# Optimization experiments

Measured on AMD Instinct MI355X. Metric: run time of the kernel, lower is better.

Reference implementation:

```python
import jax, jax.numpy as jnp
import numpy as np

B, T, C_IN, C_HID, C_EMB, K, MAX_DUR = 16, 512, 512, 256, 384, 5, 8
MAX_MEL = T * MAX_DUR  # static upper bound on regulated length (4096)
LRELU_SLOPE = 0.3
PAD = (K - 1) // 2
EPS = 1e-5


def setup_inputs() -> dict:
    key = jax.random.key(0)
    ks = jax.random.split(key, 14)
    s = 0.05
    return {
        "x": jax.random.normal(ks[0], (B, T, C_IN), jnp.float32),
        "x_res": jax.random.normal(ks[1], (B, T, C_IN), jnp.float32),
        "duration_target": jax.random.randint(ks[2], (B, T), 0, MAX_DUR, dtype=jnp.int32),
        "embeddings": jax.random.normal(ks[3], (B, T, C_EMB), jnp.float32),
        "src_mask": jnp.zeros((B, T), jnp.bool_),
        "conv1_w": s * jax.random.normal(ks[4], (K, C_IN, C_HID), jnp.float32),
        "conv1_b": jnp.zeros((C_HID,), jnp.float32),
        "ln1_g": jnp.ones((C_HID,), jnp.float32),
        "ln1_b": jnp.zeros((C_HID,), jnp.float32),
        "conv2_w": s * jax.random.normal(ks[5], (K, C_HID, C_HID), jnp.float32),
        "conv2_b": jnp.zeros((C_HID,), jnp.float32),
        "ln2_g": jnp.ones((C_HID,), jnp.float32),
        "ln2_b": jnp.zeros((C_HID,), jnp.float32),
        "lin_w": s * jax.random.normal(ks[6], (C_HID, 1), jnp.float32),
        "lin_b": jnp.zeros((1,), jnp.float32),
    }


def _conv1d(x, w, b):
    # x: [B, T, Cin], w: [K, Cin, Cout] -> [B, T, Cout] (same padding)
    y = jax.lax.conv_general_dilated(
        x, w, window_strides=(1,), padding=[(PAD, PAD)],
        dimension_numbers=("NWC", "WIO", "NWC"))
    return y + b


def _layer_norm(x, g, b):
    mu = jnp.mean(x, axis=-1, keepdims=True)
    var = jnp.mean(jnp.square(x - mu), axis=-1, keepdims=True)
    return (x - mu) * jax.lax.rsqrt(var + EPS) * g + b


def _duration_predictor(x, mask, c1w, c1b, g1, b1, c2w, c2b, g2, b2, lw, lb):
    h = jax.nn.leaky_relu(_conv1d(x, c1w, c1b), LRELU_SLOPE)
    h = _layer_norm(h, g1, b1)  # dropout is identity at eval
    h = jax.nn.leaky_relu(_conv1d(h, c2w, c2b), LRELU_SLOPE)
    h = _layer_norm(h, g2, b2)
    h = (h @ lw + lb).squeeze(-1)  # [B, T]
    return jnp.where(mask, 0.0, h)


def _length_regulate(x, duration):
    # Fused prefix-sum + gather replacement for the looped expand/cat/pad.
    # token i occupies output frames [cumsum[i-1], cumsum[i])
    cum = jnp.cumsum(duration, axis=1)              # [B, T]
    total = cum[:, -1]                              # [B] mel lengths
    pos = jnp.arange(MAX_MEL, dtype=cum.dtype)      # [MAX_MEL]
    idx = jax.vmap(lambda c: jnp.searchsorted(c, pos, side="right"))(cum)  # [B, MAX_MEL]
    idx = jnp.clip(idx, 0, duration.shape[1] - 1)
    valid = (pos[None, :] < total[:, None])         # [B, MAX_MEL]
    out = jnp.take_along_axis(x, idx[..., None], axis=1)
    out = out * valid[..., None].astype(x.dtype)    # zero-padded past mel_len
    return out, total.astype(jnp.int32)


def reference(x, x_res, duration_target, embeddings, src_mask,
              conv1_w, conv1_b, ln1_g, ln1_b, conv2_w, conv2_b, ln2_g, ln2_b,
              lin_w, lin_b):
    # upsample_train path: x_res is detached before the duration predictor
    x_res = jax.lax.stop_gradient(x_res)
    log_duration_prediction = _duration_predictor(
        x_res, src_mask, conv1_w, conv1_b, ln1_g, ln1_b,
        conv2_w, conv2_b, ln2_g, ln2_b, lin_w, lin_b)
    x_up, _ = _length_regulate(x, duration_target)
    emb_up, _ = _length_regulate(embeddings, duration_target)
    return x_up, log_duration_prediction, emb_up
```

## Files before the change

kernel.cpp:

```cpp
#include <hip/hip_runtime.h>


constexpr int Bn = 16, Tn = 512, CIN1 = 512, CHID = 256, CEMB = 384, MAXMEL = 4096;
constexpr int NROWS = Bn * Tn;
#define LRELU 0.3f
#define EPSV 1e-5f

typedef __attribute__((ext_vector_type(8))) short bf16x8;
typedef __attribute__((ext_vector_type(4))) float f32x4;
typedef __attribute__((ext_vector_type(16))) float f32x16;
typedef unsigned short ushort_t;

static __device__ __forceinline__ ushort_t f2bf(float f) {
  unsigned u = __builtin_bit_cast(unsigned, f);
  unsigned r = (u + 0x7fffu + ((u >> 16) & 1u)) >> 16;
  return (ushort_t)r;
}

__global__ __launch_bounds__(256) void wprep_kernel(const float* __restrict__ w,
                                                    ushort_t* __restrict__ out,
                                                    int CI) {
  const int gid = blockIdx.x * 256 + threadIdx.x;
  const int ksh = gid / (CI * 256);
  const int rem = gid - ksh * CI * 256;
  const int ci = rem >> 8, co = rem & 255;
  const int ci16 = ci >> 4, cob32 = co >> 5;
  const int l = ((ci >> 3) & 1) * 32 + (co & 31);
  const int j = ci & 7;
  const size_t dst = ((size_t)((ksh * (CI / 16) + ci16) * 8 + cob32)) * 512 + l * 8 + j;
  out[dst] = f2bf(w[gid]);
}

template <int CI, bool F32IN>
__global__ __launch_bounds__(256, 2) void conv_mfma_kernel(
    const float* __restrict__ xin,
    const ushort_t* __restrict__ inbf,
    const ushort_t* __restrict__ wB,
    float* __restrict__ hraw) {
  constexpr int NCHUNK = CI / 64;
  constexpr int ROWS = 36, LDSTRIDE = 72;
  __shared__ ushort_t sA[ROWS * LDSTRIDE];

  const int mt = blockIdx.x, ns = blockIdx.y;
  const int b = mt >> 4, t0 = (mt & 15) * 32;
  const int tid = threadIdx.x;
  const int l = tid & 63, nh = tid >> 6;
  const int lm = l & 31, lq = l >> 5;
  const int cob32 = ns * 4 + nh;

  f32x16 acc;
#pragma unroll
  for (int i = 0; i < 16; ++i) acc[i] = 0.f;

  const ushort_t* pB = wB + (size_t)cob32 * 512 + l * 8;

#pragma unroll 1
  for (int chunk = 0; chunk < NCHUNK; ++chunk) {
    {
      const int cibase = chunk * 64;
#pragma unroll 1
      for (int i = 0; i < 5; ++i) {
        const int p = i * 256 + tid;
        if (p < ROWS * 32) {
          const int r = p >> 5, c2 = (p & 31) * 2;
          const int t = t0 - 2 + r;
          unsigned hv = 0;
          if ((unsigned)t < (unsigned)Tn) {
            const size_t src = (size_t)(b * Tn + t) * CI + cibase + c2;
            if (F32IN) {
              const float2 v = *(const float2*)(xin + src);
              hv = (unsigned)f2bf(v.x) | ((unsigned)f2bf(v.y) << 16);
            } else {
              hv = *(const unsigned*)(inbf + src);
            }
          }
          const int sw = ((r >> 3) & 3) << 3;
          *(unsigned*)&sA[r * LDSTRIDE + (c2 ^ sw)] = hv;
        }
      }
    }
    __syncthreads();

#pragma unroll 1
    for (int ksh = 0; ksh < 5; ++ksh) {
      const int r = lm + ksh;
      const int sw = ((r >> 3) & 3) << 3;
      const size_t bbase = (size_t)((ksh * (CI / 16) + chunk * 4) * 8) * 512;
#pragma unroll
      for (int kk = 0; kk < 4; ++kk) {
        const int c = (kk * 16 + lq * 8) ^ sw;
        const bf16x8 a = *(const bf16x8*)&sA[r * LDSTRIDE + c];
        const bf16x8 bv = *(const bf16x8*)(pB + bbase + (size_t)kk * 8 * 512);
        acc = __builtin_amdgcn_mfma_f32_32x32x16_bf16(a, bv, acc, 0, 0, 0);
      }
    }
    __syncthreads();
  }

  const int col = ns * 128 + nh * 32 + lm;
  float* pOut = hraw + (size_t)(b * Tn + t0) * 256 + col;
#pragma unroll
  for (int reg = 0; reg < 16; ++reg) {
    const int row = (reg & 3) + 8 * (reg >> 2) + 4 * lq;
    pOut[(size_t)row * 256] = acc[reg];
  }
}

template <bool FINAL>
__global__ __launch_bounds__(256) void ln_kernel(
    const float* __restrict__ hraw,
    const float* __restrict__ bias, const float* __restrict__ g,
    const float* __restrict__ be, ushort_t* __restrict__ h1,
    const float* __restrict__ lw, const float* __restrict__ lb,
    const unsigned char* __restrict__ mask, float* __restrict__ ldp) {
  const int row = blockIdx.x * 4 + (threadIdx.x >> 6);
  const int l = threadIdx.x & 63;
  const f32x4 p = ((const f32x4*)hraw)[row * 64 + l];
  const f32x4 bi = ((const f32x4*)bias)[l];
  float v0 = p.x + bi.x, v1 = p.y + bi.y, v2 = p.z + bi.z, v3 = p.w + bi.w;
  v0 = (v0 > 0.f) ? v0 : LRELU * v0;
  v1 = (v1 > 0.f) ? v1 : LRELU * v1;
  v2 = (v2 > 0.f) ? v2 : LRELU * v2;
  v3 = (v3 > 0.f) ? v3 : LRELU * v3;
  float s = v0 + v1 + v2 + v3;
  float s2 = v0 * v0 + v1 * v1 + v2 * v2 + v3 * v3;
#pragma unroll
  for (int off = 32; off >= 1; off >>= 1) {
    s += __shfl_xor(s, off);
    s2 += __shfl_xor(s2, off);
  }
  const float mu = s * (1.f / 256.f);
  const float var = s2 * (1.f / 256.f) - mu * mu;
  const float rs = rsqrtf(var + EPSV);
  const f32x4 gg = ((const f32x4*)g)[l];
  const f32x4 bb = ((const f32x4*)be)[l];
  const float h0 = (v0 - mu) * rs * gg.x + bb.x;
  const float h1v = (v1 - mu) * rs * gg.y + bb.y;
  const float h2 = (v2 - mu) * rs * gg.z + bb.z;
  const float h3 = (v3 - mu) * rs * gg.w + bb.w;
  if (!FINAL) {
    ushort4 uh;
    uh.x = f2bf(h0); uh.y = f2bf(h1v); uh.z = f2bf(h2); uh.w = f2bf(h3);
    ((ushort4*)h1)[row * 64 + l] = uh;
  } else {
    const f32x4 lv = ((const f32x4*)lw)[l];
    float d = h0 * lv.x + h1v * lv.y + h2 * lv.z + h3 * lv.w;
#pragma unroll
    for (int off = 32; off >= 1; off >>= 1) d += __shfl_xor(d, off);
    if (l == 0) {
      float val = d + lb[0];
      if (mask[row]) val = 0.f;
      ldp[row] = val;
    }
  }
}

__global__ __launch_bounds__(512) void build_idx_kernel(const int* __restrict__ dur,
                                                        int* __restrict__ idx) {
  __shared__ int cum[Tn];
  const int b = blockIdx.x, t = threadIdx.x;
  const int d = dur[b * Tn + t];
  cum[t] = d;
  __syncthreads();
  for (int off = 1; off < Tn; off <<= 1) {
    int v = (t >= off) ? cum[t - off] : 0;
    __syncthreads();
    cum[t] += v;
    __syncthreads();
  }
  const int end = cum[t];
  for (int p = end - d; p < end; ++p) idx[b * MAXMEL + p] = t;
  const int total = cum[Tn - 1];
  for (int p = total + t; p < MAXMEL; p += Tn) idx[b * MAXMEL + p] = -1;
}

__global__ __launch_bounds__(256) void gather_kernel(const float* __restrict__ x,
                                                     const float* __restrict__ emb,
                                                     const int* __restrict__ idx,
                                                     float* __restrict__ x_up,
                                                     float* __restrict__ emb_up) {
  const f32x4* x4 = (const f32x4*)x;
  const f32x4* e4 = (const f32x4*)emb;
  f32x4* xu4 = (f32x4*)x_up;
  f32x4* eu4 = (f32x4*)emb_up;
  const int tid0 = blockIdx.x * 256 + threadIdx.x;
  const int stride = gridDim.x * 256;
  const f32x4 z = (f32x4){0.f, 0.f, 0.f, 0.f};
  for (int u = tid0; u < Bn * MAXMEL * 128; u += stride) {
    const int bp = u >> 7, i = u & 127;
    const int t = idx[bp];
    const int b = bp >> 12;
    const f32x4 v = (t >= 0) ? x4[((b << 9) + t) * 128 + i] : z;
    __builtin_nontemporal_store(v, &xu4[u]);
  }
  for (int u = tid0; u < Bn * MAXMEL * 96; u += stride) {
    const int bp = u / 96, i = u - bp * 96;
    const int t = idx[bp];
    const int b = bp >> 12;
    const f32x4 v = (t >= 0) ? e4[((b << 9) + t) * 96 + i] : z;
    __builtin_nontemporal_store(v, &eu4[u]);
  }
}

extern "C" void kernel_launch(void* const* d_in, const int* in_sizes, int n_in,
                              void* d_out, int out_size, void* d_ws, size_t ws_size,
                              hipStream_t stream) {
  const float* x     = (const float*)d_in[0];
  const float* x_res = (const float*)d_in[1];
  const int*   dur   = (const int*)d_in[2];
  const float* emb   = (const float*)d_in[3];
  const unsigned char* mask = (const unsigned char*)d_in[4];
  const float* c1w = (const float*)d_in[5];
  const float* c1b = (const float*)d_in[6];
  const float* g1  = (const float*)d_in[7];
  const float* b1  = (const float*)d_in[8];
  const float* c2w = (const float*)d_in[9];
  const float* c2b = (const float*)d_in[10];
  const float* g2  = (const float*)d_in[11];
  const float* b2  = (const float*)d_in[12];
  const float* lw  = (const float*)d_in[13];
  const float* lb  = (const float*)d_in[14];

  float* x_up   = (float*)d_out;
  float* ldp    = x_up + (size_t)Bn * MAXMEL * CIN1;
  float* emb_up = ldp + (size_t)Bn * Tn;

  float* hraw = emb_up;

  int* idx = (int*)d_ws;
  ushort_t* h1 = (ushort_t*)((char*)d_ws + (size_t)Bn * MAXMEL * 4);
  ushort_t* w1 = h1 + (size_t)NROWS * 256;
  ushort_t* w2 = w1 + (size_t)5 * 512 * 256;

  wprep_kernel<<<5 * 512 * 256 / 256, 256, 0, stream>>>(c1w, w1, 512);
  wprep_kernel<<<5 * 256 * 256 / 256, 256, 0, stream>>>(c2w, w2, 256);
  build_idx_kernel<<<Bn, Tn, 0, stream>>>(dur, idx);
  conv_mfma_kernel<512, true><<<dim3(256, 2), 256, 0, stream>>>(
      x_res, nullptr, w1, hraw);
  ln_kernel<false><<<NROWS / 4, 256, 0, stream>>>(
      hraw, c1b, g1, b1, h1, nullptr, nullptr, nullptr, nullptr);
  conv_mfma_kernel<256, false><<<dim3(256, 2), 256, 0, stream>>>(
      nullptr, h1, w2, hraw);
  ln_kernel<true><<<NROWS / 4, 256, 0, stream>>>(
      hraw, c2b, g2, b2, nullptr, lw, lb, mask, ldp);
  gather_kernel<<<2048, 256, 0, stream>>>(x, emb, idx, x_up, emb_up);
}
```

Before: 371.2 us.

## Merge weight prep, double conv K-chunk, and use wave-shuffle scan for indices

Combines the two weight-prep launches into one kernel where each thread writes a packed 16-byte fragment. Doubles the conv input chunk to 128 channels to halve the number of LDS fill/sync rounds. Replaces the LDS Hillis-Steele scan in index building with a wave shuffle scan plus per-wave totals. Moves the conv scratch buffer from the emb_up output into the workspace, which requires more workspace memory.

```diff
diff --git a/kernel.cpp b/kernel.cpp
--- a/kernel.cpp
+++ b/kernel.cpp
@@ -9,6 +9,7 @@
 typedef __attribute__((ext_vector_type(8))) short bf16x8;
 typedef __attribute__((ext_vector_type(4))) float f32x4;
 typedef __attribute__((ext_vector_type(16))) float f32x16;
+typedef __attribute__((ext_vector_type(4))) unsigned int u32x4;
 typedef unsigned short ushort_t;
 
 static __device__ __forceinline__ ushort_t f2bf(float f) {
@@ -17,18 +18,33 @@
   return (ushort_t)r;
 }
 
-__global__ __launch_bounds__(256) void wprep_kernel(const float* __restrict__ w,
-                                                    ushort_t* __restrict__ out,
-                                                    int CI) {
-  const int gid = blockIdx.x * 256 + threadIdx.x;
-  const int ksh = gid / (CI * 256);
-  const int rem = gid - ksh * CI * 256;
-  const int ci = rem >> 8, co = rem & 255;
-  const int ci16 = ci >> 4, cob32 = co >> 5;
-  const int l = ((ci >> 3) & 1) * 32 + (co & 31);
-  const int j = ci & 7;
-  const size_t dst = ((size_t)((ksh * (CI / 16) + ci16) * 8 + cob32)) * 512 + l * 8 + j;
-  out[dst] = f2bf(w[gid]);
+__global__ __launch_bounds__(256) void wprep_kernel(const float* __restrict__ w1src,
+                                                    const float* __restrict__ w2src,
+                                                    ushort_t* __restrict__ w1dst,
+                                                    ushort_t* __restrict__ w2dst) {
+  const int blk = blockIdx.x;
+  const float* src;
+  ushort_t* dst;
+  int CI, fr0, sh;
+  if (blk < 320) { src = w1src; dst = w1dst; CI = 512; sh = 5; fr0 = blk * 4; }
+  else           { src = w2src; dst = w2dst; CI = 256; sh = 4; fr0 = (blk - 320) * 4; }
+  const int wv = threadIdx.x >> 6, l = threadIdx.x & 63;
+  const int fr = fr0 + wv;
+  const int cob32 = fr & 7;
+  const int t = fr >> 3;
+  const int ksh = t >> sh;
+  const int ci16 = t & ((1 << sh) - 1);
+  const int ci = ci16 * 16 + (l >> 5) * 8;
+  const int co = cob32 * 32 + (l & 31);
+  ushort_t v[8];
+#pragma unroll
+  for (int j = 0; j < 8; ++j)
+    v[j] = f2bf(src[((size_t)(ksh * CI + ci + j)) * 256 + co]);
+  u32x4 pack;
+#pragma unroll
+  for (int q = 0; q < 4; ++q)
+    pack[q] = (unsigned)v[q * 2] | ((unsigned)v[q * 2 + 1] << 16);
+  *(u32x4*)&dst[(size_t)fr * 512 + l * 8] = pack;
 }
 
 template <int CI, bool F32IN>
@@ -37,8 +53,8 @@
     const ushort_t* __restrict__ inbf,
     const ushort_t* __restrict__ wB,
     float* __restrict__ hraw) {
-  constexpr int NCHUNK = CI / 64;
-  constexpr int ROWS = 36, LDSTRIDE = 72;
+  constexpr int NCHUNK = CI / 128;
+  constexpr int ROWS = 36, LDSTRIDE = 136;
   __shared__ ushort_t sA[ROWS * LDSTRIDE];
 
   const int mt = blockIdx.x, ns = blockIdx.y;
@@ -57,26 +73,24 @@
 #pragma unroll 1
   for (int chunk = 0; chunk < NCHUNK; ++chunk) {
     {
-      const int cibase = chunk * 64;
+      const int cibase = chunk * 128;
 #pragma unroll 1
-      for (int i = 0; i < 5; ++i) {
+      for (int i = 0; i < 9; ++i) {
         const int p = i * 256 + tid;
-        if (p < ROWS * 32) {
-          const int r = p >> 5, c2 = (p & 31) * 2;
-          const int t = t0 - 2 + r;
-          unsigned hv = 0;
-          if ((unsigned)t < (unsigned)Tn) {
-            const size_t src = (size_t)(b * Tn + t) * CI + cibase + c2;
-            if (F32IN) {
-              const float2 v = *(const float2*)(xin + src);
-              hv = (unsigned)f2bf(v.x) | ((unsigned)f2bf(v.y) << 16);
-            } else {
-              hv = *(const unsigned*)(inbf + src);
-            }
+        const int r = p >> 6, c2 = (p & 63) * 2;
+        const int t = t0 - 2 + r;
+        unsigned hv = 0;
+        if ((unsigned)t < (unsigned)Tn) {
+          const size_t src = (size_t)(b * Tn + t) * CI + cibase + c2;
+          if (F32IN) {
+            const float2 v = *(const float2*)(xin + src);
+            hv = (unsigned)f2bf(v.x) | ((unsigned)f2bf(v.y) << 16);
+          } else {
+            hv = *(const unsigned*)(inbf + src);
           }
-          const int sw = ((r >> 3) & 3) << 3;
-          *(unsigned*)&sA[r * LDSTRIDE + (c2 ^ sw)] = hv;
         }
+        const int sw = ((r >> 3) & 3) << 3;
+        *(unsigned*)&sA[r * LDSTRIDE + (c2 ^ sw)] = hv;
       }
     }
     __syncthreads();
@@ -85,9 +99,9 @@
     for (int ksh = 0; ksh < 5; ++ksh) {
       const int r = lm + ksh;
       const int sw = ((r >> 3) & 3) << 3;
-      const size_t bbase = (size_t)((ksh * (CI / 16) + chunk * 4) * 8) * 512;
-#pragma unroll
-      for (int kk = 0; kk < 4; ++kk) {
+      const size_t bbase = (size_t)((ksh * (CI / 16) + chunk * 8) * 8) * 512;
+#pragma unroll
+      for (int kk = 0; kk < 8; ++kk) {
         const int c = (kk * 16 + lq * 8) ^ sw;
         const bf16x8 a = *(const bf16x8*)&sA[r * LDSTRIDE + c];
         const bf16x8 bv = *(const bf16x8*)(pB + bbase + (size_t)kk * 8 * 512);
@@ -157,21 +171,28 @@
 
 __global__ __launch_bounds__(512) void build_idx_kernel(const int* __restrict__ dur,
                                                         int* __restrict__ idx) {
-  __shared__ int cum[Tn];
-  const int b = blockIdx.x, t = threadIdx.x;
-  const int d = dur[b * Tn + t];
-  cum[t] = d;
+  __shared__ int wsum[8];
+  const int b = blockIdx.x, tid = threadIdx.x;
+  const int lane = tid & 63, wv = tid >> 6;
+  const int d = dur[b * Tn + tid];
+  int v = d;
+#pragma unroll
+  for (int off = 1; off <= 32; off <<= 1) {
+    const int t = __shfl_up(v, off);
+    if (lane >= off) v += t;
+  }
+  if (lane == 63) wsum[wv] = v;
   __syncthreads();
-  for (int off = 1; off < Tn; off <<= 1) {
-    int v = (t >= off) ? cum[t - off] : 0;
-    __syncthreads();
-    cum[t] += v;
-    __syncthreads();
-  }
-  const int end = cum[t];
-  for (int p = end - d; p < end; ++p) idx[b * MAXMEL + p] = t;
-  const int total = cum[Tn - 1];
-  for (int p = total + t; p < MAXMEL; p += Tn) idx[b * MAXMEL + p] = -1;
+  int woff = 0, total = 0;
+#pragma unroll
+  for (int i = 0; i < 8; ++i) {
+    const int s = wsum[i];
+    if (i < wv) woff += s;
+    total += s;
+  }
+  const int end = v + woff;
+  for (int p = end - d; p < end; ++p) idx[b * MAXMEL + p] = tid;
+  for (int p = total + tid; p < MAXMEL; p += 512) idx[b * MAXMEL + p] = -1;
 }
 
 __global__ __launch_bounds__(256) void gather_kernel(const float* __restrict__ x,
@@ -225,16 +246,14 @@
   float* ldp    = x_up + (size_t)Bn * MAXMEL * CIN1;
   float* emb_up = ldp + (size_t)Bn * Tn;
 
-  float* hraw = emb_up;
-
   int* idx = (int*)d_ws;
   ushort_t* h1 = (ushort_t*)((char*)d_ws + (size_t)Bn * MAXMEL * 4);
   ushort_t* w1 = h1 + (size_t)NROWS * 256;
   ushort_t* w2 = w1 + (size_t)5 * 512 * 256;
-
-  wprep_kernel<<<5 * 512 * 256 / 256, 256, 0, stream>>>(c1w, w1, 512);
-  wprep_kernel<<<5 * 256 * 256 / 256, 256, 0, stream>>>(c2w, w2, 256);
-  build_idx_kernel<<<Bn, Tn, 0, stream>>>(dur, idx);
+  float* hraw = (float*)(w2 + (size_t)5 * 256 * 256);
+
+  wprep_kernel<<<480, 256, 0, stream>>>(c1w, c2w, w1, w2);
+  build_idx_kernel<<<Bn, 512, 0, stream>>>(dur, idx);
   conv_mfma_kernel<512, true><<<dim3(256, 2), 256, 0, stream>>>(
       x_res, nullptr, w1, hraw);
   ln_kernel<false><<<NROWS / 4, 256, 0, stream>>>(
```

Measured after the change: 359.7 us. -3.1%, faster.
